# Optimization experiments

Hardware: AMD Instinct MI355X
Metric: run time of the kernel (lower is better)

## Reference

```python
import jax, jax.numpy as jnp
import numpy as np

HEAD_DIM = 128
NUM_HEADS = 16
HIDDEN = 2048
SEQ = 4096
ROPE_THETA = 10000.0
RMS_EPS = 1e-6


def _rms_norm(x, w, eps=RMS_EPS):
    # per-head RMSNorm over last dim (head_dim)
    var = jnp.mean(jnp.square(x), axis=-1, keepdims=True)
    return x * jax.lax.rsqrt(var + eps) * w


def _rope_cos_sin(position_ids, dim=HEAD_DIM, theta=ROPE_THETA):
    freqs = 1.0 / theta ** (jnp.arange(0, dim, 2, dtype=jnp.float32) / dim)  # [dim/2]
    ang = position_ids.astype(jnp.float32)[:, None] * freqs[None, :]  # [S, dim/2]
    return jnp.cos(ang), jnp.sin(ang)


def _apply_rope(x, cos, sin):
    # x: [S, H, D]; pairs (x0, x1) along last dim act as complex numbers
    S, H, D = x.shape
    xr = x.astype(jnp.float32).reshape(S, H, D // 2, 2)
    x0, x1 = xr[..., 0], xr[..., 1]
    c = cos[:, None, :]  # [S, 1, D/2]
    s = sin[:, None, :]
    o0 = x0 * c - x1 * s
    o1 = x0 * s + x1 * c
    out = jnp.stack((o0, o1), axis=-1).reshape(S, H, D)
    return out.astype(x.dtype)


def setup_inputs() -> dict:
    key = jax.random.key(0)
    ks = jax.random.split(key, 8)
    std = 0.02
    return {
        "hidden_states": jax.random.normal(ks[0], (SEQ, HIDDEN), dtype=jnp.float32),
        "position_ids": jnp.arange(SEQ, dtype=jnp.int64 if jax.config.jax_enable_x64 else jnp.int32),
        "wq": jax.random.normal(ks[1], (HIDDEN, HIDDEN), dtype=jnp.float32) * std,
        "wk": jax.random.normal(ks[2], (HIDDEN, HIDDEN), dtype=jnp.float32) * std,
        "wv": jax.random.normal(ks[3], (HIDDEN, HIDDEN), dtype=jnp.float32) * std,
        "wo": jax.random.normal(ks[4], (HIDDEN, HIDDEN), dtype=jnp.float32) * std,
        "q_norm_w": jnp.ones((HEAD_DIM,), dtype=jnp.float32),
        "k_norm_w": jnp.ones((HEAD_DIM,), dtype=jnp.float32),
    }


def reference(hidden_states, position_ids, wq, wk, wv, wo, q_norm_w, k_norm_w):
    S = hidden_states.shape[0]
    # QKV projections (NormalLinear: x @ weight)
    xq = hidden_states @ wq
    xk = hidden_states @ wk
    xv = hidden_states @ wv
    # split heads: [S, H, D]
    xq = xq.reshape(S, NUM_HEADS, HEAD_DIM)
    xk = xk.reshape(S, NUM_HEADS, HEAD_DIM)
    xv = xv.reshape(S, NUM_HEADS, HEAD_DIM)
    # per-head qk RMSNorm
    xq = _rms_norm(xq, q_norm_w)
    xk = _rms_norm(xk, k_norm_w)
    # rotary embedding
    cos, sin = _rope_cos_sin(position_ids)
    xq = _apply_rope(xq, cos, sin)
    xk = _apply_rope(xk, cos, sin)
    # scaled dot-product attention (no mask), TNH layout
    context = jax.nn.dot_product_attention(xq, xk, xv)
    # merge heads and output projection (dropout p=0 -> identity)
    out = context.reshape(S, NUM_HEADS * HEAD_DIM) @ wo
    return out
```

## Files before the change

kernel.cpp:

```cpp
#include <hip/hip_runtime.h>

typedef __bf16 bf16x8 __attribute__((ext_vector_type(8)));
typedef __bf16 bf16x4 __attribute__((ext_vector_type(4)));
typedef float  f32x4  __attribute__((ext_vector_type(4)));

#define MFMA16(A, B, C) __builtin_amdgcn_mfma_f32_16x16x32_bf16(A, B, C, 0, 0, 0)
#define AS1 __attribute__((address_space(1)))
#define AS3 __attribute__((address_space(3)))

#if __has_builtin(__builtin_amdgcn_exp2f)
#define EXP2F(x) __builtin_amdgcn_exp2f(x)
#else
#define EXP2F(x) exp2f(x)
#endif

__global__ __launch_bounds__(256) void prep(const float* __restrict__ hs,
                                            const float* __restrict__ wq,
                                            const float* __restrict__ wk,
                                            const float* __restrict__ wv,
                                            const float* __restrict__ wo,
                                            __bf16* __restrict__ xb,
                                            __bf16* __restrict__ wqkvtb,
                                            __bf16* __restrict__ wotb) {
    __shared__ float tile[32][33];
    const int z = blockIdx.z;
    const int tx = threadIdx.x, ty = threadIdx.y;
    if (z == 4) {
        const int t = ty * 32 + tx;
        size_t bid = (size_t)blockIdx.y * 64 + blockIdx.x;
        size_t base = bid * 2048 + t * 4;
        for (int c = 0; c < 2; ++c) {
            float4 v = *(const float4*)(hs + base + c * 1024);
            bf16x4 o;
            o.x = (__bf16)v.x; o.y = (__bf16)v.y; o.z = (__bf16)v.z; o.w = (__bf16)v.w;
            *(bf16x4*)(xb + base + c * 1024) = o;
        }
        return;
    }
    const float* src = (z == 0) ? wq : (z == 1) ? wk : (z == 2) ? wv : wo;
    __bf16* dst = (z < 3) ? (wqkvtb + (size_t)z * 2048 * 2048) : wotb;
    int x0 = blockIdx.x * 32, y0 = blockIdx.y * 32;
    for (int r = 0; r < 4; ++r)
        tile[ty + 8 * r][tx] = src[(size_t)(y0 + ty + 8 * r) * 2048 + x0 + tx];
    __syncthreads();
    for (int r = 0; r < 4; ++r)
        dst[(size_t)(x0 + ty + 8 * r) * 2048 + y0 + tx] = (__bf16)tile[tx][ty + 8 * r];
}

__global__ __launch_bounds__(256) void rope_vt(const __bf16* __restrict__ qkv,
                                               const float* __restrict__ qw,
                                               const float* __restrict__ kw,
                                               const int* __restrict__ pos_ids,
                                               __bf16* __restrict__ qhb,
                                               __bf16* __restrict__ khb,
                                               __bf16* __restrict__ vtb) {
    __shared__ __bf16 tile[32][33];
    if (blockIdx.y < 32) {
        int u = threadIdx.x >> 6, lane = threadIdx.x & 63;
        int s = blockIdx.x * 4 + u;
        int slot = blockIdx.y;
        bool isQ = slot < 16;
        int h = slot & 15;
        size_t base = (size_t)s * 6144 + (isQ ? 0 : 2048) + h * 128 + lane * 2;
        float x0 = (float)qkv[base], x1 = (float)qkv[base + 1];
        float ss = x0 * x0 + x1 * x1;
        for (int m = 1; m < 64; m <<= 1) ss += __shfl_xor(ss, m);
        float rr = rsqrtf(ss * (1.0f / 128.0f) + 1e-6f);
        const float* wp = isQ ? qw : kw;
        float n0 = x0 * rr * wp[lane * 2], n1 = x1 * rr * wp[lane * 2 + 1];
        float freq = EXP2F(-(float)lane * 0.2076205059004571f);
        float ang = (float)pos_ids[s] * freq;
        float sn, cs;
        sincosf(ang, &sn, &cs);
        float o0 = n0 * cs - n1 * sn;
        float o1 = n0 * sn + n1 * cs;
        if (isQ) { o0 *= 0.12751744416196178f; o1 *= 0.12751744416196178f; }
        __bf16* dst = (isQ ? qhb : khb) + (size_t)h * 4096 * 128 + (size_t)s * 128 + lane * 2;
        dst[0] = (__bf16)o0; dst[1] = (__bf16)o1;
    } else {
        int linear = (blockIdx.y - 32) * 1024 + blockIdx.x;
        int h = linear >> 9, rem = linear & 511;
        int s0 = (rem & 127) * 32, d0 = (rem >> 7) * 32;
        int tx = threadIdx.x & 31, ty = threadIdx.x >> 5;
        for (int r = 0; r < 4; ++r)
            tile[ty + 8 * r][tx] = qkv[(size_t)(s0 + ty + 8 * r) * 6144 + 4096 + h * 128 + d0 + tx];
        __syncthreads();
        for (int r = 0; r < 4; ++r)
            vtb[(size_t)h * 128 * 4096 + (size_t)(d0 + ty + 8 * r) * 4096 + s0 + tx] = tile[tx][ty + 8 * r];
    }
}

template <bool F32OUT>
__global__ __launch_bounds__(256) void gemm_bt(const __bf16* __restrict__ A, int lda,
                                               const __bf16* __restrict__ Bt, int ldb,
                                               void* __restrict__ Cout, int ldc, int K) {
    __shared__ __bf16 as[3][128][32];
    __shared__ __bf16 bs[3][128][32];
    const int m0 = blockIdx.x * 128, n0 = blockIdx.y * 128;
    const int t = threadIdx.x;
    const int lane = t & 63, w = t >> 6;
    const int wm = (w >> 1) * 64, wn = (w & 1) * 64;
    const int ln = lane & 15, quad = lane >> 4;
    auto as3 = (AS3 uint32_t*)&as[0][0][0];
    auto bs3 = (AS3 uint32_t*)&bs[0][0][0];
    f32x4 acc[4][4] = {};

#define G_STAGE(buf, k0)                                                             \
    for (int c = 0; c < 2; ++c) {                                                    \
        int g = c * 256 + t;                                                         \
        int row = g >> 2, kc = g & 3;                                                \
        __builtin_amdgcn_global_load_lds(                                            \
            (const AS1 uint32_t*)&A[(size_t)(m0 + row) * lda + (k0) + kc * 8],       \
            as3 + (buf) * 2048 + c * 1024 + w * 256, 16, 0, 0);                      \
        __builtin_amdgcn_global_load_lds(                                            \
            (const AS1 uint32_t*)&Bt[(size_t)(n0 + row) * ldb + (k0) + kc * 8],      \
            bs3 + (buf) * 2048 + c * 1024 + w * 256, 16, 0, 0);                      \
    }

    const int nk = K >> 5;
    G_STAGE(0, 0)
    G_STAGE(1, 32)
    for (int kt = 0; kt < nk; ++kt) {
        const int nxt = kt + 2;
        if (nxt < nk) {
            G_STAGE(nxt % 3, nxt * 32)
            asm volatile("s_waitcnt vmcnt(8)" ::: "memory");
        } else if (nxt == nk) {
            asm volatile("s_waitcnt vmcnt(4)" ::: "memory");
        } else {
            asm volatile("s_waitcnt vmcnt(0)" ::: "memory");
        }
        __builtin_amdgcn_s_barrier();
        const int b = kt % 3;
        bf16x8 af[4], bfr[4];
        for (int i = 0; i < 4; ++i) af[i] = *(const bf16x8*)&as[b][wm + i * 16 + ln][quad * 8];
        for (int j = 0; j < 4; ++j) bfr[j] = *(const bf16x8*)&bs[b][wn + j * 16 + ln][quad * 8];
        for (int i = 0; i < 4; ++i)
            for (int j = 0; j < 4; ++j)
                acc[i][j] = MFMA16(af[i], bfr[j], acc[i][j]);
        __builtin_amdgcn_s_barrier();
    }
#undef G_STAGE

    for (int i = 0; i < 4; ++i)
        for (int j = 0; j < 4; ++j)
            for (int r = 0; r < 4; ++r) {
                int row = m0 + wm + i * 16 + quad * 4 + r;
                int col = n0 + wn + j * 16 + ln;
                if (F32OUT) ((float*)Cout)[(size_t)row * ldc + col] = acc[i][j][r];
                else        ((__bf16*)Cout)[(size_t)row * ldc + col] = (__bf16)acc[i][j][r];
            }
}

__global__ __launch_bounds__(256) void flash_attn(const __bf16* __restrict__ Q,
                                                  const __bf16* __restrict__ Kb,
                                                  const __bf16* __restrict__ Vt,
                                                  __bf16* __restrict__ ctx) {
    __shared__ __bf16 kbuf[2][64][128];
    __shared__ __bf16 vbuf[2][128][64];
    __shared__ __bf16 ps[4][32][64];

    int bid = blockIdx.x + (int)gridDim.x * blockIdx.y;
    int swz = (bid & 7) * 64 + (bid >> 3);
    const int h  = swz >> 5;
    const int m0 = (swz & 31) * 128;

    const int t = threadIdx.x;
    const int lane = t & 63, w = t >> 6;
    const int ln = lane & 15, quad = lane >> 4;
    const __bf16* Qh = Q + (size_t)h * 4096 * 128;
    const __bf16* Kh = Kb + (size_t)h * 4096 * 128;
    const __bf16* Vh = Vt + (size_t)h * 128 * 4096;

    const int kcc = (t & 15) ^ ((t >> 4) & 7);
    const int vcc = (t & 7) ^ ((t >> 3) & 7);
    auto kb3 = (AS3 uint32_t*)&kbuf[0][0][0];
    auto vb3 = (AS3 uint32_t*)&vbuf[0][0][0];
    const char* kbase = (const char*)&kbuf[0][0][0];
    const char* vbase = (const char*)&vbuf[0][0][0];

    bf16x8 qf[2][4];
    for (int half = 0; half < 2; ++half) {
        for (int i = 0; i < 4; ++i) {
            int row = (t >> 4) + i * 16;
            *(uint4*)&kbuf[0][row][(t & 15) * 8] =
                *(const uint4*)&Qh[(size_t)(m0 + half * 64 + row) * 128 + kcc * 8];
        }
        __syncthreads();
        int r = w * 16 + ln;
        for (int kk = 0; kk < 4; ++kk)
            qf[half][kk] = *(const bf16x8*)(kbase + r * 256 + ((((kk * 4 + quad) ^ (ln & 7)) << 4)));
        __syncthreads();
    }

#define STAGE_KV(buf, tile)                                                          \
    for (int i = 0; i < 4; ++i) {                                                    \
        int krow = (t >> 4) + i * 16;                                                \
        __builtin_amdgcn_global_load_lds(                                            \
            (const AS1 uint32_t*)&Kh[(size_t)((tile) * 64 + krow) * 128 + kcc * 8],  \
            kb3 + (buf) * 4096 + (w * 64 + i * 256) * 4, 16, 0, 0);                  \
        int vrow = (t >> 3) + i * 32;                                                \
        __builtin_amdgcn_global_load_lds(                                            \
            (const AS1 uint32_t*)&Vh[(size_t)vrow * 4096 + (tile) * 64 + vcc * 8],   \
            vb3 + (buf) * 4096 + (w * 64 + i * 256) * 4, 16, 0, 0);                  \
    }

    STAGE_KV(0, 0)
    __syncthreads();

    f32x4 oacc[2][8] = {};
    float rs[2][4] = {};
    int cur = 0;

    for (int kb = 0; kb < 64; ++kb) {
        if (kb + 1 < 64) { STAGE_KV(cur ^ 1, kb + 1) }

        const char* ksb = kbase + cur * 16384;
        const char* vsb = vbase + cur * 16384;

        f32x4 sacc[2][4];
        const f32x4 mC = {-16.5f, -16.5f, -16.5f, -16.5f};
        for (int i = 0; i < 2; ++i)
            for (int j = 0; j < 4; ++j) sacc[i][j] = mC;
        for (int j = 0; j < 4; ++j)
            for (int kk = 0; kk < 4; ++kk) {
                bf16x8 kf = *(const bf16x8*)(ksb + (j * 16 + ln) * 256 +
                                             (((kk * 4 + quad) ^ (ln & 7)) << 4));
                sacc[0][j] = MFMA16(qf[0][kk], kf, sacc[0][j]);
                sacc[1][j] = MFMA16(qf[1][kk], kf, sacc[1][j]);
            }

        for (int i = 0; i < 2; ++i)
            for (int j = 0; j < 4; ++j)
                for (int r = 0; r < 4; ++r) {
                    float p = EXP2F(sacc[i][j][r]);
                    rs[i][r] += p;
                    int prow = i * 16 + quad * 4 + r;
                    ps[w][prow][(j * 16 + ln) ^ ((prow & 7) << 3)] = (__bf16)p;
                }

        bf16x8 pf[2][2];
        for (int i = 0; i < 2; ++i)
            for (int kk = 0; kk < 2; ++kk)
                pf[i][kk] = *(const bf16x8*)&ps[w][i * 16 + ln][(kk * 32 + quad * 8) ^ ((ln & 7) << 3)];
        for (int t8 = 0; t8 < 8; ++t8)
            for (int kk = 0; kk < 2; ++kk) {
                bf16x8 vf = *(const bf16x8*)(vsb + (t8 * 16 + ln) * 128 +
                                             (((kk * 4 + quad) ^ (ln & 7)) << 4));
                oacc[0][t8] = MFMA16(pf[0][kk], vf, oacc[0][t8]);
                oacc[1][t8] = MFMA16(pf[1][kk], vf, oacc[1][t8]);
            }
        __syncthreads();
        cur ^= 1;
    }
#undef STAGE_KV

    float inv[2][4];
    for (int i = 0; i < 2; ++i)
        for (int r = 0; r < 4; ++r) {
            float s = rs[i][r];
            for (int msk = 1; msk < 16; msk <<= 1) s += __shfl_xor(s, msk);
            inv[i][r] = 1.0f / s;
        }
    for (int i = 0; i < 2; ++i)
        for (int t8 = 0; t8 < 8; ++t8)
            for (int r = 0; r < 4; ++r) {
                int row = m0 + i * 64 + w * 16 + quad * 4 + r;
                int col = h * 128 + t8 * 16 + ln;
                ctx[(size_t)row * 2048 + col] = (__bf16)(oacc[i][t8][r] * inv[i][r]);
            }
}

extern "C" void kernel_launch(void* const* d_in, const int* in_sizes, int n_in,
                              void* d_out, int out_size, void* d_ws, size_t ws_size,
                              hipStream_t stream) {
    const float* hs  = (const float*)d_in[0];
    const int*   pos = (const int*)d_in[1];
    const float* wq  = (const float*)d_in[2];
    const float* wk  = (const float*)d_in[3];
    const float* wv  = (const float*)d_in[4];
    const float* wo  = (const float*)d_in[5];
    const float* qw  = (const float*)d_in[6];
    const float* kw  = (const float*)d_in[7];

    char* ws = (char*)d_ws;
    const size_t MB = 1024 * 1024;
    __bf16* xb     = (__bf16*)(ws + 0);
    __bf16* wqkvtb = (__bf16*)(ws + 16 * MB);
    __bf16* qhb    = (__bf16*)(ws + 0);
    __bf16* khb    = (__bf16*)(ws + 16 * MB);
    __bf16* vtb    = (__bf16*)(ws + 32 * MB);
    __bf16* qkvb   = (__bf16*)(ws + 48 * MB);
    __bf16* ctxb   = (__bf16*)(ws + 48 * MB);
    __bf16* wotb   = (__bf16*)(ws + 96 * MB);

    prep<<<dim3(64, 64, 5), dim3(32, 8), 0, stream>>>(hs, wq, wk, wv, wo, xb, wqkvtb, wotb);

    gemm_bt<false><<<dim3(32, 48), 256, 0, stream>>>(xb, 2048, wqkvtb, 2048, qkvb, 6144, 2048);

    rope_vt<<<dim3(1024, 40), 256, 0, stream>>>(qkvb, qw, kw, pos, qhb, khb, vtb);

    flash_attn<<<dim3(32, 16), 256, 0, stream>>>(qhb, khb, vtb, ctxb);

    gemm_bt<true><<<dim3(32, 16), 256, 0, stream>>>(ctxb, 2048, wotb, 2048, d_out, 2048, 2048);
}
```

Measured before the change: 494.3 us.

## Switch flash attention to 32x32 MFMA with register-resident P via permlane swap

Rewrites the attention inner loop to use 32x32x16 bf16 MFMAs, computing S transposed (K as A operand) so each lane holds a column of scores. Probabilities are packed to bf16 and rearranged across lane halves with permlane32_swap, which removes the LDS round trip for P and its shared buffer. It also adds s_setprio around the MFMA sections and reduces row sums through a small LDS array at the end. The output tiling changes so each wave owns 32 query rows, which changes register pressure and how K and V fragments are reused.

```diff
diff --git a/kernel.cpp b/kernel.cpp
--- a/kernel.cpp
+++ b/kernel.cpp
@@ -3,8 +3,11 @@
 typedef __bf16 bf16x8 __attribute__((ext_vector_type(8)));
 typedef __bf16 bf16x4 __attribute__((ext_vector_type(4)));
 typedef float  f32x4  __attribute__((ext_vector_type(4)));
+typedef float  f32x16 __attribute__((ext_vector_type(16)));
+typedef unsigned u32x4 __attribute__((ext_vector_type(4)));
 
 #define MFMA16(A, B, C) __builtin_amdgcn_mfma_f32_16x16x32_bf16(A, B, C, 0, 0, 0)
+#define MFMA32(A, B, C) __builtin_amdgcn_mfma_f32_32x32x16_bf16(A, B, C, 0, 0, 0)
 #define AS1 __attribute__((address_space(1)))
 #define AS3 __attribute__((address_space(3)))
 
@@ -13,6 +16,12 @@
 #else
 #define EXP2F(x) exp2f(x)
 #endif
+
+__device__ __forceinline__ unsigned pk_bf16(float lo, float hi) {
+    unsigned l = (unsigned)__builtin_bit_cast(unsigned short, (__bf16)lo);
+    unsigned h = (unsigned)__builtin_bit_cast(unsigned short, (__bf16)hi);
+    return l | (h << 16);
+}
 
 __global__ __launch_bounds__(256) void prep(const float* __restrict__ hs,
                                             const float* __restrict__ wq,
@@ -152,13 +161,45 @@
             }
 }
 
+#define SOFTMAX_PV(sac, ktv)                                                        \
+    {                                                                               \
+        float p[16];                                                                \
+        _Pragma("unroll")                                                           \
+        for (int r = 0; r < 16; ++r) { p[r] = EXP2F((sac)[r]); rs += p[r]; }        \
+        unsigned a00 = pk_bf16(p[0], p[1]),  a01 = pk_bf16(p[2], p[3]);             \
+        unsigned b00 = pk_bf16(p[4], p[5]),  b01 = pk_bf16(p[6], p[7]);             \
+        unsigned a10 = pk_bf16(p[8], p[9]),  a11 = pk_bf16(p[10], p[11]);           \
+        unsigned b10 = pk_bf16(p[12], p[13]), b11 = pk_bf16(p[14], p[15]);          \
+        auto s00 = __builtin_amdgcn_permlane32_swap(a00, b00, false, false);        \
+        auto s01 = __builtin_amdgcn_permlane32_swap(a01, b01, false, false);        \
+        auto s10 = __builtin_amdgcn_permlane32_swap(a10, b10, false, false);        \
+        auto s11 = __builtin_amdgcn_permlane32_swap(a11, b11, false, false);        \
+        u32x4 w0, w1;                                                               \
+        w0[0] = s00[0]; w0[1] = s01[0]; w0[2] = s00[1]; w0[3] = s01[1];             \
+        w1[0] = s10[0]; w1[1] = s11[0]; w1[2] = s10[1]; w1[3] = s11[1];             \
+        bf16x8 pf0 = __builtin_bit_cast(bf16x8, w0);                                \
+        bf16x8 pf1 = __builtin_bit_cast(bf16x8, w1);                                \
+        __builtin_amdgcn_s_setprio(1);                                              \
+        _Pragma("unroll")                                                           \
+        for (int dt = 0; dt < 4; ++dt) {                                            \
+            int vrow = dt * 32 + q32;                                               \
+            int co0 = (((ktv) * 2 + 0) << 1) | hi;                                  \
+            int co1 = (((ktv) * 2 + 1) << 1) | hi;                                  \
+            bf16x8 vf0 = *(const bf16x8*)(vsb + vrow * 128 + ((co0 ^ (q32 & 7)) << 4)); \
+            bf16x8 vf1 = *(const bf16x8*)(vsb + vrow * 128 + ((co1 ^ (q32 & 7)) << 4)); \
+            oacc[dt] = MFMA32(pf0, vf0, oacc[dt]);                                  \
+            oacc[dt] = MFMA32(pf1, vf1, oacc[dt]);                                  \
+        }                                                                           \
+        __builtin_amdgcn_s_setprio(0);                                              \
+    }
+
 __global__ __launch_bounds__(256) void flash_attn(const __bf16* __restrict__ Q,
                                                   const __bf16* __restrict__ Kb,
                                                   const __bf16* __restrict__ Vt,
                                                   __bf16* __restrict__ ctx) {
     __shared__ __bf16 kbuf[2][64][128];
     __shared__ __bf16 vbuf[2][128][64];
-    __shared__ __bf16 ps[4][32][64];
+    __shared__ float lred[4][32];
 
     int bid = blockIdx.x + (int)gridDim.x * blockIdx.y;
     int swz = (bid & 7) * 64 + (bid >> 3);
@@ -167,7 +208,7 @@
 
     const int t = threadIdx.x;
     const int lane = t & 63, w = t >> 6;
-    const int ln = lane & 15, quad = lane >> 4;
+    const int q32 = lane & 31, hi = lane >> 5;
     const __bf16* Qh = Q + (size_t)h * 4096 * 128;
     const __bf16* Kh = Kb + (size_t)h * 4096 * 128;
     const __bf16* Vh = Vt + (size_t)h * 128 * 4096;
@@ -179,7 +220,7 @@
     const char* kbase = (const char*)&kbuf[0][0][0];
     const char* vbase = (const char*)&vbuf[0][0][0];
 
-    bf16x8 qf[2][4];
+    bf16x8 qf[8];
     for (int half = 0; half < 2; ++half) {
         for (int i = 0; i < 4; ++i) {
             int row = (t >> 4) + i * 16;
@@ -187,9 +228,12 @@
                 *(const uint4*)&Qh[(size_t)(m0 + half * 64 + row) * 128 + kcc * 8];
         }
         __syncthreads();
-        int r = w * 16 + ln;
-        for (int kk = 0; kk < 4; ++kk)
-            qf[half][kk] = *(const bf16x8*)(kbase + r * 256 + ((((kk * 4 + quad) ^ (ln & 7)) << 4)));
+        if ((w >> 1) == half) {
+            int r = (w & 1) * 32 + q32;
+            #pragma unroll
+            for (int dc = 0; dc < 8; ++dc)
+                qf[dc] = *(const bf16x8*)(kbase + r * 256 + ((((dc << 1) | hi) ^ (r & 7)) << 4));
+        }
         __syncthreads();
     }
 
@@ -208,8 +252,8 @@
     STAGE_KV(0, 0)
     __syncthreads();
 
-    f32x4 oacc[2][8] = {};
-    float rs[2][4] = {};
+    f32x16 oacc[4] = {};
+    float rs = 0.0f;
     int cur = 0;
 
     for (int kb = 0; kb < 64; ++kb) {
@@ -218,57 +262,43 @@
         const char* ksb = kbase + cur * 16384;
         const char* vsb = vbase + cur * 16384;
 
-        f32x4 sacc[2][4];
-        const f32x4 mC = {-16.5f, -16.5f, -16.5f, -16.5f};
-        for (int i = 0; i < 2; ++i)
-            for (int j = 0; j < 4; ++j) sacc[i][j] = mC;
-        for (int j = 0; j < 4; ++j)
-            for (int kk = 0; kk < 4; ++kk) {
-                bf16x8 kf = *(const bf16x8*)(ksb + (j * 16 + ln) * 256 +
-                                             (((kk * 4 + quad) ^ (ln & 7)) << 4));
-                sacc[0][j] = MFMA16(qf[0][kk], kf, sacc[0][j]);
-                sacc[1][j] = MFMA16(qf[1][kk], kf, sacc[1][j]);
-            }
-
-        for (int i = 0; i < 2; ++i)
-            for (int j = 0; j < 4; ++j)
-                for (int r = 0; r < 4; ++r) {
-                    float p = EXP2F(sacc[i][j][r]);
-                    rs[i][r] += p;
-                    int prow = i * 16 + quad * 4 + r;
-                    ps[w][prow][(j * 16 + ln) ^ ((prow & 7) << 3)] = (__bf16)p;
-                }
-
-        bf16x8 pf[2][2];
-        for (int i = 0; i < 2; ++i)
-            for (int kk = 0; kk < 2; ++kk)
-                pf[i][kk] = *(const bf16x8*)&ps[w][i * 16 + ln][(kk * 32 + quad * 8) ^ ((ln & 7) << 3)];
-        for (int t8 = 0; t8 < 8; ++t8)
-            for (int kk = 0; kk < 2; ++kk) {
-                bf16x8 vf = *(const bf16x8*)(vsb + (t8 * 16 + ln) * 128 +
-                                             (((kk * 4 + quad) ^ (ln & 7)) << 4));
-                oacc[0][t8] = MFMA16(pf[0][kk], vf, oacc[0][t8]);
-                oacc[1][t8] = MFMA16(pf[1][kk], vf, oacc[1][t8]);
-            }
+        f32x16 sacc0, sacc1;
+        #pragma unroll
+        for (int e = 0; e < 16; ++e) { sacc0[e] = -16.5f; sacc1[e] = -16.5f; }
+        __builtin_amdgcn_s_setprio(1);
+        #pragma unroll
+        for (int dc = 0; dc < 8; ++dc) {
+            int co = (dc << 1) | hi;
+            bf16x8 kf0 = *(const bf16x8*)(ksb + q32 * 256        + ((co ^ (q32 & 7)) << 4));
+            bf16x8 kf1 = *(const bf16x8*)(ksb + (32 + q32) * 256 + ((co ^ (q32 & 7)) << 4));
+            sacc0 = MFMA32(kf0, qf[dc], sacc0);
+            sacc1 = MFMA32(kf1, qf[dc], sacc1);
+        }
+        __builtin_amdgcn_s_setprio(0);
+
+        SOFTMAX_PV(sacc0, 0)
+        SOFTMAX_PV(sacc1, 1)
+
         __syncthreads();
         cur ^= 1;
     }
 #undef STAGE_KV
 
-    float inv[2][4];
-    for (int i = 0; i < 2; ++i)
-        for (int r = 0; r < 4; ++r) {
-            float s = rs[i][r];
-            for (int msk = 1; msk < 16; msk <<= 1) s += __shfl_xor(s, msk);
-            inv[i][r] = 1.0f / s;
-        }
-    for (int i = 0; i < 2; ++i)
-        for (int t8 = 0; t8 < 8; ++t8)
-            for (int r = 0; r < 4; ++r) {
-                int row = m0 + i * 64 + w * 16 + quad * 4 + r;
-                int col = h * 128 + t8 * 16 + ln;
-                ctx[(size_t)row * 2048 + col] = (__bf16)(oacc[i][t8][r] * inv[i][r]);
-            }
+    float rt = rs + __shfl_xor(rs, 32);
+    if (hi == 0) lred[w][q32] = rt;
+    __syncthreads();
+    float inv[16];
+    #pragma unroll
+    for (int r = 0; r < 16; ++r)
+        inv[r] = 1.0f / lred[w][(r & 3) + 8 * (r >> 2) + 4 * hi];
+    #pragma unroll
+    for (int dt = 0; dt < 4; ++dt)
+        #pragma unroll
+        for (int r = 0; r < 16; ++r) {
+            int row = m0 + w * 32 + (r & 3) + 8 * (r >> 2) + 4 * hi;
+            int col = h * 128 + dt * 32 + q32;
+            ctx[(size_t)row * 2048 + col] = (__bf16)(oacc[dt][r] * inv[r]);
+        }
 }
 
 extern "C" void kernel_launch(void* const* d_in, const int* in_sizes, int n_in,
```

Result: no change. 496.8 us (+0.5%).
